# Optimization experiments

Measured on AMD Instinct MI355X. Metric: run time of the kernel, lower is better.

## Reference

```python
import jax, jax.numpy as jnp
import numpy as np

DIM = 1024
H = 16
HD = DIM // H
HIDDEN = 4096
EPS = 1e-5


def layer_norm(x, w, b):
    mu = jnp.mean(x, axis=-1, keepdims=True)
    var = jnp.mean(jnp.square(x - mu), axis=-1, keepdims=True)
    return (x - mu) * jax.lax.rsqrt(var + EPS) * w + b


def setup_inputs() -> dict:
    key = jax.random.key(0)
    ks = jax.random.split(key, 12)
    B, N = 4, 1024
    s = 0.02
    return {
        "x": jax.random.normal(ks[0], (B, N, DIM), jnp.float32),
        "rel_pos_bias": jax.random.normal(ks[1], (H, N, N), jnp.float32) * 0.1,
        "attn_mask": jax.random.randint(ks[2], (B, N), 0, 2, jnp.int32),
        "norm1_w": jnp.ones((DIM,), jnp.float32),
        "norm1_b": jnp.zeros((DIM,), jnp.float32),
        "qkv_w": jax.random.normal(ks[3], (3 * DIM, DIM), jnp.float32) * s,
        "q_bias": jnp.zeros((DIM,), jnp.float32),
        "v_bias": jnp.zeros((DIM,), jnp.float32),
        "proj_w": jax.random.normal(ks[4], (DIM, DIM), jnp.float32) * s,
        "proj_b": jnp.zeros((DIM,), jnp.float32),
        "norm2_w": jnp.ones((DIM,), jnp.float32),
        "norm2_b": jnp.zeros((DIM,), jnp.float32),
        "mlp_w1": jax.random.normal(ks[5], (HIDDEN, DIM), jnp.float32) * s,
        "mlp_b1": jnp.zeros((HIDDEN,), jnp.float32),
        "mlp_w2": jax.random.normal(ks[6], (DIM, HIDDEN), jnp.float32) * s,
        "mlp_b2": jnp.zeros((DIM,), jnp.float32),
    }


def attention(x, rel_pos_bias, attn_mask, qkv_w, q_bias, v_bias, proj_w, proj_b):
    B, N, C = x.shape
    scale = HD ** (-0.5)
    qkv_bias = jnp.concatenate([q_bias, jnp.zeros_like(v_bias), v_bias])
    qkv = x @ qkv_w.T + qkv_bias  # [B,N,3C]
    qkv = qkv.reshape(B, N, 3, H, HD).transpose(2, 0, 3, 1, 4)  # [3,B,H,N,hd]
    q, k, v = qkv[0] * scale, qkv[1], qkv[2]
    attn = jnp.einsum("bhqd,bhkd->bhqk", q, k) + rel_pos_bias[None]
    mask = attn_mask.astype(bool)[:, None, None, :]  # key padding mask
    attn = jnp.where(mask, attn, -jnp.inf)
    attn = jax.nn.softmax(attn, axis=-1)
    out = jnp.einsum("bhqk,bhkd->bhqd", attn, v)
    out = out.transpose(0, 2, 1, 3).reshape(B, N, C)
    return out @ proj_w.T + proj_b


def mlp(x, w1, b1, w2, b2):
    h = jax.nn.gelu(x @ w1.T + b1, approximate=False)
    return h @ w2.T + b2


def reference(x, rel_pos_bias, attn_mask, norm1_w, norm1_b, qkv_w, q_bias, v_bias,
              proj_w, proj_b, norm2_w, norm2_b, mlp_w1, mlp_b1, mlp_w2, mlp_b2):
    # pre-norm block, gamma=None, postnorm=False
    x = x + attention(layer_norm(x, norm1_w, norm1_b), rel_pos_bias, attn_mask,
                      qkv_w, q_bias, v_bias, proj_w, proj_b)
    x = x + mlp(layer_norm(x, norm2_w, norm2_b), mlp_w1, mlp_b1, mlp_w2, mlp_b2)
    return x
```

## Files before the change

### kernel.cpp

```cpp
#include <hip/hip_runtime.h>
#include <math.h>

#define DIM 1024
#define NHEAD 16
#define HD 64
#define HIDDEN 4096
#define SEQ 1024
#define BATCH 4
#define ROWS (BATCH*SEQ)

typedef __attribute__((ext_vector_type(8))) short bf16x8;
typedef __attribute__((ext_vector_type(4))) float f32x4;
typedef __attribute__((ext_vector_type(4))) unsigned short us4;

__device__ __forceinline__ unsigned short f2bf(float f) {
  unsigned u = __builtin_bit_cast(unsigned, f);
  u += 0x7fffu + ((u >> 16) & 1u);
  return (unsigned short)(u >> 16);
}

__device__ __forceinline__ void glds16(const void* g, void* l) {
  __builtin_amdgcn_global_load_lds((const __attribute__((address_space(1))) void*)g,
                                   (__attribute__((address_space(3))) void*)l,
                                   16, 0, 0);
}

__global__ void cvt_all(const float* __restrict__ a, const float* __restrict__ b,
                        const float* __restrict__ c, const float* __restrict__ d,
                        unsigned short* __restrict__ oa, unsigned short* __restrict__ ob,
                        unsigned short* __restrict__ oc, unsigned short* __restrict__ od) {
  const int na = 3 * DIM * DIM / 4, nb = DIM * DIM / 4, nc = HIDDEN * DIM / 4, nd = DIM * HIDDEN / 4;
  const int total = na + nb + nc + nd;
  for (int i = blockIdx.x * blockDim.x + threadIdx.x; i < total; i += gridDim.x * blockDim.x) {
    const float* in; unsigned short* out; int j = i;
    if (j < na)             { in = a; out = oa; }
    else if ((j -= na) < nb){ in = b; out = ob; }
    else if ((j -= nb) < nc){ in = c; out = oc; }
    else                    { j -= nc; in = d; out = od; }
    float4 v = reinterpret_cast<const float4*>(in)[j];
    us4 o = { f2bf(v.x), f2bf(v.y), f2bf(v.z), f2bf(v.w) };
    reinterpret_cast<us4*>(out)[j] = o;
  }
}

__global__ void ln_kernel(const float* __restrict__ x, const float* __restrict__ w,
                          const float* __restrict__ b, unsigned short* __restrict__ out) {
  int row = blockIdx.x;
  const float* xr = x + (size_t)row * DIM;
  int t = threadIdx.x;
  float4 v = *reinterpret_cast<const float4*>(xr + t * 4);
  float s  = v.x + v.y + v.z + v.w;
  float s2 = v.x*v.x + v.y*v.y + v.z*v.z + v.w*v.w;
#pragma unroll
  for (int m = 1; m < 64; m <<= 1) { s += __shfl_xor(s, m); s2 += __shfl_xor(s2, m); }
  __shared__ float red[8];
  int wv = t >> 6, ln = t & 63;
  if (ln == 0) { red[wv] = s; red[4 + wv] = s2; }
  __syncthreads();
  s  = red[0] + red[1] + red[2] + red[3];
  s2 = red[4] + red[5] + red[6] + red[7];
  float mu  = s * (1.0f / DIM);
  float var = s2 * (1.0f / DIM) - mu * mu;
  float rs  = rsqrtf(var + 1e-5f);
  float4 wv4 = *reinterpret_cast<const float4*>(w + t * 4);
  float4 bv4 = *reinterpret_cast<const float4*>(b + t * 4);
  us4 o = { f2bf((v.x - mu) * rs * wv4.x + bv4.x),
            f2bf((v.y - mu) * rs * wv4.y + bv4.y),
            f2bf((v.z - mu) * rs * wv4.z + bv4.z),
            f2bf((v.w - mu) * rs * wv4.w + bv4.w) };
  *reinterpret_cast<us4*>(out + (size_t)row * DIM + t * 4) = o;
}

template<int MODE, int BN>
__global__ __launch_bounds__(256)
void gemm128(const unsigned short* __restrict__ A, const unsigned short* __restrict__ Bw,
             int K, int N,
             const float* __restrict__ bias, const float* __restrict__ resid,
             float* __restrict__ outf, unsigned short* __restrict__ outh,
             unsigned short* __restrict__ qo, unsigned short* __restrict__ ko,
             unsigned short* __restrict__ vto,
             const float* __restrict__ qbias, const float* __restrict__ vbias)
{
  constexpr int NJ = BN / 32;
  __shared__ unsigned short smA[2][128 * 32];
  __shared__ unsigned short smB[2][BN * 32];
  const int tid = threadIdx.x;
  const int wv = tid >> 6, ln = tid & 63;
  const int tile_m = blockIdx.x * 128, tile_n = blockIdx.y * BN;
  const int wm = (wv >> 1) * 64, wn = (wv & 1) * (BN / 2);

  const unsigned short* gA = A  + (size_t)(tile_m + wv * 32 + (ln >> 2)) * K + (ln & 3) * 8;
  const unsigned short* gB = Bw + (size_t)(tile_n + wv * (BN / 4) + (ln >> 2)) * K + (ln & 3) * 8;

  f32x4 acc[4][NJ] = {};
  const int lr = ln & 15, lc8 = (ln >> 4) * 8;

  auto stage = [&](int buf, int k0) {
    glds16(gA + k0,                  &smA[buf][wv * 1024]);
    glds16(gA + k0 + 16 * (size_t)K, &smA[buf][wv * 1024 + 512]);
    glds16(gB + k0,                  &smB[buf][wv * (BN / 4) * 32]);
    if (BN == 128) glds16(gB + k0 + 16 * (size_t)K, &smB[buf][wv * 1024 + 512]);
  };

  stage(0, 0);
  __syncthreads();
  int cur = 0;
  for (int k0 = 0; k0 < K; k0 += 32) {
    if (k0 + 32 < K) stage(cur ^ 1, k0 + 32);
    bf16x8 af[4], bfr[NJ];
#pragma unroll
    for (int i = 0; i < 4; i++)
      af[i] = *reinterpret_cast<const bf16x8*>(&smA[cur][(wm + i * 16 + lr) * 32 + lc8]);
#pragma unroll
    for (int j = 0; j < NJ; j++)
      bfr[j] = *reinterpret_cast<const bf16x8*>(&smB[cur][(wn + j * 16 + lr) * 32 + lc8]);
#pragma unroll
    for (int i = 0; i < 4; i++)
#pragma unroll
      for (int j = 0; j < NJ; j++)
        acc[i][j] = __builtin_amdgcn_mfma_f32_16x16x32_bf16(af[i], bfr[j], acc[i][j], 0, 0, 0);
    __syncthreads();
    cur ^= 1;
  }

  const int lcol = ln & 15, lrow4 = (ln >> 4) * 4;
#pragma unroll
  for (int i = 0; i < 4; i++) {
#pragma unroll
    for (int j = 0; j < NJ; j++) {
      int gm0 = tile_m + wm + i * 16 + lrow4;
      int gn  = tile_n + wn + j * 16 + lcol;
#pragma unroll
      for (int r = 0; r < 4; r++) {
        int gm = gm0 + r;
        float val = acc[i][j][r];
        if (MODE == 0) {
          int b = gm >> 10, n = gm & 1023;
          if (gn < DIM) {
            float q = (val + qbias[gn]) * 0.125f;
            qo[(size_t)((b * NHEAD + (gn >> 6)) * SEQ + n) * HD + (gn & 63)] = f2bf(q);
          } else if (gn < 2 * DIM) {
            int g2 = gn - DIM;
            ko[(size_t)((b * NHEAD + (g2 >> 6)) * SEQ + n) * HD + (g2 & 63)] = f2bf(val);
          } else {
            int g3 = gn - 2 * DIM;
            vto[(size_t)((b * NHEAD + (g3 >> 6)) * HD + (g3 & 63)) * SEQ + n] = f2bf(val + vbias[g3]);
          }
        } else if (MODE == 1) {
          outf[(size_t)gm * N + gn] = val + bias[gn] + resid[(size_t)gm * N + gn];
        } else if (MODE == 2) {
          float t = val + bias[gn];
          float g = 0.5f * t * (1.0f + erff(t * 0.70710678118f));
          outh[(size_t)gm * N + gn] = f2bf(g);
        } else {
          outf[(size_t)gm * N + gn] = val + bias[gn] + resid[(size_t)gm * N + gn];
        }
      }
    }
  }
}

__global__ __launch_bounds__(512)
void attn_kernel(const unsigned short* __restrict__ qg, const unsigned short* __restrict__ kg,
                 const unsigned short* __restrict__ vtg, const float* __restrict__ rpb,
                 const int* __restrict__ amask, unsigned short* __restrict__ outh)
{
  constexpr int PSTR = 72;
  __shared__ unsigned short smK[2][64 * 64];
  __shared__ unsigned short smV[2][64 * 64];
  __shared__ unsigned short pls[8][16 * PSTR];
  const int tid = threadIdx.x;
  const int wv = tid >> 6, ln = tid & 63;
  const int bh = blockIdx.y, b = bh >> 4, h = bh & 15;
  const int q0 = blockIdx.x * 128 + wv * 16;
  const unsigned short* qb = qg  + (size_t)bh * SEQ * HD;
  const unsigned short* kb = kg  + (size_t)bh * SEQ * HD;
  const unsigned short* vb = vtg + (size_t)bh * HD * SEQ;
  const int* mp = amask + b * SEQ;
  unsigned short* myp = pls[wv];

  const int lcol = ln & 15, g = ln >> 4, lc8 = g * 8, lrow4 = g * 4;
  const int sw = (lcol & 7) << 3;
  const float* bprow = rpb + (size_t)h * SEQ * SEQ + (size_t)(q0 + lcol) * SEQ;

  const int srr = ln >> 3;
  const int scc = (ln & 7) ^ srr;

  bf16x8 aq0 = *reinterpret_cast<const bf16x8*>(qb + (size_t)(q0 + lcol) * HD + lc8);
  bf16x8 aq1 = *reinterpret_cast<const bf16x8*>(qb + (size_t)(q0 + lcol) * HD + 32 + lc8);

  f32x4 o[4] = {};
  float m = -1e30f, l = 0.f;

  auto stage = [&](int buf, int kt) {
    int row = wv * 8 + srr;
    glds16(kb + (size_t)(kt + row) * HD + scc * 8, &smK[buf][wv * 512]);
    glds16(vb + (size_t)row * SEQ + kt + scc * 8, &smV[buf][wv * 512]);
  };

  stage(0, 0);
  __syncthreads();

  for (int t = 0; t < SEQ / 64; t++) {
    const int cur = t & 1;
    const int kt = t * 64;
    float4 bv4[4]; int4 mv[4];
#pragma unroll
    for (int j = 0; j < 4; j++) {
      bv4[j] = *reinterpret_cast<const float4*>(bprow + kt + j * 16 + lrow4);
      mv[j]  = *reinterpret_cast<const int4*>(mp + kt + j * 16 + lrow4);
    }
    if (t < SEQ / 64 - 1) stage(cur ^ 1, kt + 64);

    f32x4 s[4];
#pragma unroll
    for (int j = 0; j < 4; j++) {
      int r = j * 16 + lcol;
      bf16x8 bk0 = *reinterpret_cast<const bf16x8*>(&smK[cur][r * 64 + (lc8 ^ sw)]);
      bf16x8 bk1 = *reinterpret_cast<const bf16x8*>(&smK[cur][r * 64 + ((32 + lc8) ^ sw)]);
      f32x4 z = {0.f, 0.f, 0.f, 0.f};
      z = __builtin_amdgcn_mfma_f32_16x16x32_bf16(bk0, aq0, z, 0, 0, 0);
      z = __builtin_amdgcn_mfma_f32_16x16x32_bf16(bk1, aq1, z, 0, 0, 0);
      s[j] = z;
    }
#pragma unroll
    for (int j = 0; j < 4; j++) {
      s[j][0] = mv[j].x ? s[j][0] + bv4[j].x : -1e30f;
      s[j][1] = mv[j].y ? s[j][1] + bv4[j].y : -1e30f;
      s[j][2] = mv[j].z ? s[j][2] + bv4[j].z : -1e30f;
      s[j][3] = mv[j].w ? s[j][3] + bv4[j].w : -1e30f;
    }
    float pm = fmaxf(fmaxf(fmaxf(s[0][0], s[0][1]), fmaxf(s[0][2], s[0][3])),
                     fmaxf(fmaxf(s[1][0], s[1][1]), fmaxf(s[1][2], s[1][3])));
    pm = fmaxf(pm, fmaxf(fmaxf(fmaxf(s[2][0], s[2][1]), fmaxf(s[2][2], s[2][3])),
                         fmaxf(fmaxf(s[3][0], s[3][1]), fmaxf(s[3][2], s[3][3]))));
    pm = fmaxf(pm, __shfl_xor(pm, 16));
    pm = fmaxf(pm, __shfl_xor(pm, 32));
    float mn = fmaxf(m, pm);
    float fr = __expf(m - mn);
    m = mn;
    float rs = 0.f;
#pragma unroll
    for (int j = 0; j < 4; j++)
#pragma unroll
      for (int r = 0; r < 4; r++) {
        float p = __expf(s[j][r] - m);
        s[j][r] = p;
        rs += p;
      }
    rs += __shfl_xor(rs, 16);
    rs += __shfl_xor(rs, 32);
    l = l * fr + rs;
    float frq[4];
#pragma unroll
    for (int r = 0; r < 4; r++) frq[r] = __shfl(fr, lrow4 + r);
#pragma unroll
    for (int d = 0; d < 4; d++)
#pragma unroll
      for (int r = 0; r < 4; r++) o[d][r] *= frq[r];
#pragma unroll
    for (int j = 0; j < 4; j++) {
      us4 po = { f2bf(s[j][0]), f2bf(s[j][1]), f2bf(s[j][2]), f2bf(s[j][3]) };
      *reinterpret_cast<us4*>(myp + lcol * PSTR + j * 16 + lrow4) = po;
    }
    asm volatile("s_waitcnt lgkmcnt(0)" ::: "memory");
    __builtin_amdgcn_sched_barrier(0);
#pragma unroll
    for (int c = 0; c < 2; c++) {
      bf16x8 ap = *reinterpret_cast<const bf16x8*>(myp + lcol * PSTR + c * 32 + lc8);
#pragma unroll
      for (int d = 0; d < 4; d++) {
        int vr = d * 16 + lcol;
        bf16x8 bvv = *reinterpret_cast<const bf16x8*>(&smV[cur][vr * 64 + ((c * 32 + lc8) ^ sw)]);
        o[d] = __builtin_amdgcn_mfma_f32_16x16x32_bf16(ap, bvv, o[d], 0, 0, 0);
      }
    }
    __syncthreads();
  }
  float linv = 1.0f / l;
  float lq[4];
#pragma unroll
  for (int r = 0; r < 4; r++) lq[r] = __shfl(linv, lrow4 + r);
#pragma unroll
  for (int d = 0; d < 4; d++)
#pragma unroll
    for (int r = 0; r < 4; r++)
      outh[(size_t)(b * SEQ + q0 + lrow4 + r) * DIM + h * HD + d * 16 + lcol] = f2bf(o[d][r] * lq[r]);
}

extern "C" void kernel_launch(void* const* d_in, const int* in_sizes, int n_in,
                              void* d_out, int out_size, void* d_ws, size_t ws_size,
                              hipStream_t stream)
{
  const float* x      = (const float*)d_in[0];
  const float* rpb    = (const float*)d_in[1];
  const int*   amask  = (const int*)d_in[2];
  const float* n1w    = (const float*)d_in[3];
  const float* n1b    = (const float*)d_in[4];
  const float* qkv_w  = (const float*)d_in[5];
  const float* q_bias = (const float*)d_in[6];
  const float* v_bias = (const float*)d_in[7];
  const float* proj_w = (const float*)d_in[8];
  const float* proj_b = (const float*)d_in[9];
  const float* n2w    = (const float*)d_in[10];
  const float* n2b    = (const float*)d_in[11];
  const float* w1     = (const float*)d_in[12];
  const float* b1     = (const float*)d_in[13];
  const float* w2     = (const float*)d_in[14];
  const float* b2     = (const float*)d_in[15];
  float* out = (float*)d_out;

  char* ws = (char*)d_ws;
  size_t off = 0;
  auto alloc = [&](size_t bytes) { char* p = ws + off; off += (bytes + 255) & ~(size_t)255; return p; };
  unsigned short* xn1    = (unsigned short*)alloc((size_t)ROWS * DIM * 2);
  unsigned short* xn2    = (unsigned short*)alloc((size_t)ROWS * DIM * 2);
  unsigned short* wqkv_h = (unsigned short*)alloc((size_t)3 * DIM * DIM * 2);
  unsigned short* wproj_h= (unsigned short*)alloc((size_t)DIM * DIM * 2);
  unsigned short* w1_h   = (unsigned short*)alloc((size_t)HIDDEN * DIM * 2);
  unsigned short* w2_h   = (unsigned short*)alloc((size_t)DIM * HIDDEN * 2);
  unsigned short* qh     = (unsigned short*)alloc((size_t)ROWS * DIM * 2);
  unsigned short* kh     = (unsigned short*)alloc((size_t)ROWS * DIM * 2);
  unsigned short* vth    = (unsigned short*)alloc((size_t)ROWS * DIM * 2);
  unsigned short* attn_h = (unsigned short*)alloc((size_t)ROWS * DIM * 2);
  float*          xres   = (float*)alloc((size_t)ROWS * DIM * 4);
  unsigned short* hmid   = (unsigned short*)alloc((size_t)ROWS * HIDDEN * 2);

  cvt_all<<<2048, 256, 0, stream>>>(qkv_w, proj_w, w1, w2, wqkv_h, wproj_h, w1_h, w2_h);

  ln_kernel<<<ROWS, 256, 0, stream>>>(x, n1w, n1b, xn1);
  gemm128<0, 128><<<dim3(ROWS / 128, 3 * DIM / 128), 256, 0, stream>>>(
      xn1, wqkv_h, DIM, 3 * DIM, nullptr, nullptr, nullptr, nullptr, qh, kh, vth, q_bias, v_bias);
  attn_kernel<<<dim3(SEQ / 128, BATCH * NHEAD), 512, 0, stream>>>(qh, kh, vth, rpb, amask, attn_h);
  gemm128<1, 64><<<dim3(ROWS / 128, DIM / 64), 256, 0, stream>>>(
      attn_h, wproj_h, DIM, DIM, proj_b, x, xres, nullptr, nullptr, nullptr, nullptr, nullptr, nullptr);
  ln_kernel<<<ROWS, 256, 0, stream>>>(xres, n2w, n2b, xn2);
  gemm128<2, 128><<<dim3(ROWS / 128, HIDDEN / 128), 256, 0, stream>>>(
      xn2, w1_h, DIM, HIDDEN, b1, nullptr, nullptr, hmid, nullptr, nullptr, nullptr, nullptr, nullptr);
  gemm128<3, 64><<<dim3(ROWS / 128, DIM / 64), 256, 0, stream>>>(
      hmid, w2_h, HIDDEN, DIM, b2, xres, out, nullptr, nullptr, nullptr, nullptr, nullptr, nullptr);
}
```

Baseline: 308.4 us.

## Triple-buffer GEMM loads and prefetch attention bias/mask one tile ahead

The GEMM moves from double to triple LDS buffering. It issues loads two k-steps ahead and replaces the per-iteration __syncthreads with one s_barrier plus explicit vmcnt waits, so global_load_lds traffic overlaps more MFMA work. The attention kernel now prefetches the next tile's rel-pos bias and mask into registers, drops the trailing __syncthreads in favour of a barrier at the top of the loop, and raises wave priority around the MFMA sections. One risk: the vmcnt wait follows the barrier, so a wave only waits on its own loads before reading LDS that other waves staged, which may be a cross-wave race. The extra buffer also adds LDS and register pressure.

```diff
diff --git a/kernel.cpp b/kernel.cpp
--- a/kernel.cpp
+++ b/kernel.cpp
@@ -82,8 +82,9 @@
              const float* __restrict__ qbias, const float* __restrict__ vbias)
 {
   constexpr int NJ = BN / 32;
-  __shared__ unsigned short smA[2][128 * 32];
-  __shared__ unsigned short smB[2][BN * 32];
+  constexpr int GL = (BN == 128) ? 4 : 3;
+  __shared__ unsigned short smA[3][128 * 32];
+  __shared__ unsigned short smB[3][BN * 32];
   const int tid = threadIdx.x;
   const int wv = tid >> 6, ln = tid & 63;
   const int tile_m = blockIdx.x * 128, tile_n = blockIdx.y * BN;
@@ -103,10 +104,21 @@
   };
 
   stage(0, 0);
-  __syncthreads();
+  stage(1, 32);
   int cur = 0;
   for (int k0 = 0; k0 < K; k0 += 32) {
-    if (k0 + 32 < K) stage(cur ^ 1, k0 + 32);
+    __builtin_amdgcn_s_barrier();
+    __builtin_amdgcn_sched_barrier(0);
+    if (k0 + 64 < K) {
+      int nb = cur - 1; if (nb < 0) nb += 3;
+      stage(nb, k0 + 64);
+      asm volatile("s_waitcnt vmcnt(%0)" :: "i"(2 * GL) : "memory");
+    } else if (k0 + 32 < K) {
+      asm volatile("s_waitcnt vmcnt(%0)" :: "i"(GL) : "memory");
+    } else {
+      asm volatile("s_waitcnt vmcnt(0)" ::: "memory");
+    }
+    __builtin_amdgcn_sched_barrier(0);
     bf16x8 af[4], bfr[NJ];
 #pragma unroll
     for (int i = 0; i < 4; i++)
@@ -119,8 +131,7 @@
 #pragma unroll
       for (int j = 0; j < NJ; j++)
         acc[i][j] = __builtin_amdgcn_mfma_f32_16x16x32_bf16(af[i], bfr[j], acc[i][j], 0, 0, 0);
-    __syncthreads();
-    cur ^= 1;
+    cur = (cur == 2) ? 0 : cur + 1;
   }
 
   const int lcol = ln & 15, lrow4 = (ln >> 4) * 4;
@@ -166,6 +177,7 @@
                  const int* __restrict__ amask, unsigned short* __restrict__ outh)
 {
   constexpr int PSTR = 72;
+  constexpr int NT = SEQ / 64;
   __shared__ unsigned short smK[2][64 * 64];
   __shared__ unsigned short smV[2][64 * 64];
   __shared__ unsigned short pls[8][16 * PSTR];
@@ -198,21 +210,36 @@
     glds16(vb + (size_t)row * SEQ + kt + scc * 8, &smV[buf][wv * 512]);
   };
 
+  float4 bcur[4]; int4 mcur[4];
+  float4 bnxt[4]; int4 mnxt[4];
+
   stage(0, 0);
-  __syncthreads();
-
-  for (int t = 0; t < SEQ / 64; t++) {
+#pragma unroll
+  for (int j = 0; j < 4; j++) {
+    bcur[j] = *reinterpret_cast<const float4*>(bprow + j * 16 + lrow4);
+    mcur[j] = *reinterpret_cast<const int4*>(mp + j * 16 + lrow4);
+  }
+
+  for (int t = 0; t < NT; t++) {
     const int cur = t & 1;
     const int kt = t * 64;
-    float4 bv4[4]; int4 mv[4];
-#pragma unroll
-    for (int j = 0; j < 4; j++) {
-      bv4[j] = *reinterpret_cast<const float4*>(bprow + kt + j * 16 + lrow4);
-      mv[j]  = *reinterpret_cast<const int4*>(mp + kt + j * 16 + lrow4);
-    }
-    if (t < SEQ / 64 - 1) stage(cur ^ 1, kt + 64);
+    __builtin_amdgcn_s_barrier();
+    __builtin_amdgcn_sched_barrier(0);
+    if (t + 1 < NT) {
+      stage(cur ^ 1, kt + 64);
+#pragma unroll
+      for (int j = 0; j < 4; j++) {
+        bnxt[j] = *reinterpret_cast<const float4*>(bprow + kt + 64 + j * 16 + lrow4);
+        mnxt[j] = *reinterpret_cast<const int4*>(mp + kt + 64 + j * 16 + lrow4);
+      }
+      asm volatile("s_waitcnt vmcnt(10)" ::: "memory");
+    } else {
+      asm volatile("s_waitcnt vmcnt(0)" ::: "memory");
+    }
+    __builtin_amdgcn_sched_barrier(0);
 
     f32x4 s[4];
+    __builtin_amdgcn_s_setprio(1);
 #pragma unroll
     for (int j = 0; j < 4; j++) {
       int r = j * 16 + lcol;
@@ -223,12 +250,13 @@
       z = __builtin_amdgcn_mfma_f32_16x16x32_bf16(bk1, aq1, z, 0, 0, 0);
       s[j] = z;
     }
+    __builtin_amdgcn_s_setprio(0);
 #pragma unroll
     for (int j = 0; j < 4; j++) {
-      s[j][0] = mv[j].x ? s[j][0] + bv4[j].x : -1e30f;
-      s[j][1] = mv[j].y ? s[j][1] + bv4[j].y : -1e30f;
-      s[j][2] = mv[j].z ? s[j][2] + bv4[j].z : -1e30f;
-      s[j][3] = mv[j].w ? s[j][3] + bv4[j].w : -1e30f;
+      s[j][0] = mcur[j].x ? s[j][0] + bcur[j].x : -1e30f;
+      s[j][1] = mcur[j].y ? s[j][1] + bcur[j].y : -1e30f;
+      s[j][2] = mcur[j].z ? s[j][2] + bcur[j].z : -1e30f;
+      s[j][3] = mcur[j].w ? s[j][3] + bcur[j].w : -1e30f;
     }
     float pm = fmaxf(fmaxf(fmaxf(s[0][0], s[0][1]), fmaxf(s[0][2], s[0][3])),
                      fmaxf(fmaxf(s[1][0], s[1][1]), fmaxf(s[1][2], s[1][3])));
@@ -265,6 +293,7 @@
     }
     asm volatile("s_waitcnt lgkmcnt(0)" ::: "memory");
     __builtin_amdgcn_sched_barrier(0);
+    __builtin_amdgcn_s_setprio(1);
 #pragma unroll
     for (int c = 0; c < 2; c++) {
       bf16x8 ap = *reinterpret_cast<const bf16x8*>(myp + lcol * PSTR + c * 32 + lc8);
@@ -275,7 +304,11 @@
         o[d] = __builtin_amdgcn_mfma_f32_16x16x32_bf16(ap, bvv, o[d], 0, 0, 0);
       }
     }
-    __syncthreads();
+    __builtin_amdgcn_s_setprio(0);
+    if (t + 1 < NT) {
+#pragma unroll
+      for (int j = 0; j < 4; j++) { bcur[j] = bnxt[j]; mcur[j] = mnxt[j]; }
+    }
   }
   float linv = 1.0f / l;
   float lq[4];
```

Result: slower. 331.2 us (+7.4%).

## Load attention K/V fragments directly from global memory and skip rescales lazily

Applied to the files above, without the earlier changes.

The attention kernel stops staging K and V tiles in LDS with double buffering and block barriers. Each wave now loads its K and V MFMA fragments straight from global memory into registers, and the block shrinks to 4 waves covering 64 queries. It also adds lazy online-softmax rescaling that skips the max update and output rescale when the new max exceeds the old by at most 8, and uses s_setprio around the MFMA sections. This removes the LDS traffic and __syncthreads, but each wave now re-reads K/V from global or L2 with less reuse across the block.

```diff
diff --git a/kernel.cpp b/kernel.cpp
--- a/kernel.cpp
+++ b/kernel.cpp
@@ -160,19 +160,17 @@
   }
 }
 
-__global__ __launch_bounds__(512)
+__global__ __launch_bounds__(256)
 void attn_kernel(const unsigned short* __restrict__ qg, const unsigned short* __restrict__ kg,
                  const unsigned short* __restrict__ vtg, const float* __restrict__ rpb,
                  const int* __restrict__ amask, unsigned short* __restrict__ outh)
 {
   constexpr int PSTR = 72;
-  __shared__ unsigned short smK[2][64 * 64];
-  __shared__ unsigned short smV[2][64 * 64];
-  __shared__ unsigned short pls[8][16 * PSTR];
+  __shared__ unsigned short pls[4][16 * PSTR];
   const int tid = threadIdx.x;
   const int wv = tid >> 6, ln = tid & 63;
   const int bh = blockIdx.y, b = bh >> 4, h = bh & 15;
-  const int q0 = blockIdx.x * 128 + wv * 16;
+  const int q0 = blockIdx.x * 64 + wv * 16;
   const unsigned short* qb = qg  + (size_t)bh * SEQ * HD;
   const unsigned short* kb = kg  + (size_t)bh * SEQ * HD;
   const unsigned short* vb = vtg + (size_t)bh * HD * SEQ;
@@ -180,11 +178,7 @@
   unsigned short* myp = pls[wv];
 
   const int lcol = ln & 15, g = ln >> 4, lc8 = g * 8, lrow4 = g * 4;
-  const int sw = (lcol & 7) << 3;
   const float* bprow = rpb + (size_t)h * SEQ * SEQ + (size_t)(q0 + lcol) * SEQ;
-
-  const int srr = ln >> 3;
-  const int scc = (ln & 7) ^ srr;
 
   bf16x8 aq0 = *reinterpret_cast<const bf16x8*>(qb + (size_t)(q0 + lcol) * HD + lc8);
   bf16x8 aq1 = *reinterpret_cast<const bf16x8*>(qb + (size_t)(q0 + lcol) * HD + 32 + lc8);
@@ -192,37 +186,33 @@
   f32x4 o[4] = {};
   float m = -1e30f, l = 0.f;
 
-  auto stage = [&](int buf, int kt) {
-    int row = wv * 8 + srr;
-    glds16(kb + (size_t)(kt + row) * HD + scc * 8, &smK[buf][wv * 512]);
-    glds16(vb + (size_t)row * SEQ + kt + scc * 8, &smV[buf][wv * 512]);
-  };
-
-  stage(0, 0);
-  __syncthreads();
-
-  for (int t = 0; t < SEQ / 64; t++) {
-    const int cur = t & 1;
-    const int kt = t * 64;
+  for (int kt = 0; kt < SEQ; kt += 64) {
+    bf16x8 kf0[4], kf1[4];
     float4 bv4[4]; int4 mv[4];
 #pragma unroll
     for (int j = 0; j < 4; j++) {
+      const unsigned short* kp = kb + (size_t)(kt + j * 16 + lcol) * HD + lc8;
+      kf0[j] = *reinterpret_cast<const bf16x8*>(kp);
+      kf1[j] = *reinterpret_cast<const bf16x8*>(kp + 32);
       bv4[j] = *reinterpret_cast<const float4*>(bprow + kt + j * 16 + lrow4);
       mv[j]  = *reinterpret_cast<const int4*>(mp + kt + j * 16 + lrow4);
     }
-    if (t < SEQ / 64 - 1) stage(cur ^ 1, kt + 64);
-
     f32x4 s[4];
+    __builtin_amdgcn_s_setprio(1);
 #pragma unroll
     for (int j = 0; j < 4; j++) {
-      int r = j * 16 + lcol;
-      bf16x8 bk0 = *reinterpret_cast<const bf16x8*>(&smK[cur][r * 64 + (lc8 ^ sw)]);
-      bf16x8 bk1 = *reinterpret_cast<const bf16x8*>(&smK[cur][r * 64 + ((32 + lc8) ^ sw)]);
       f32x4 z = {0.f, 0.f, 0.f, 0.f};
-      z = __builtin_amdgcn_mfma_f32_16x16x32_bf16(bk0, aq0, z, 0, 0, 0);
-      z = __builtin_amdgcn_mfma_f32_16x16x32_bf16(bk1, aq1, z, 0, 0, 0);
+      z = __builtin_amdgcn_mfma_f32_16x16x32_bf16(kf0[j], aq0, z, 0, 0, 0);
+      z = __builtin_amdgcn_mfma_f32_16x16x32_bf16(kf1[j], aq1, z, 0, 0, 0);
       s[j] = z;
     }
+    __builtin_amdgcn_s_setprio(0);
+    bf16x8 vf[2][4];
+#pragma unroll
+    for (int c = 0; c < 2; c++)
+#pragma unroll
+      for (int d = 0; d < 4; d++)
+        vf[c][d] = *reinterpret_cast<const bf16x8*>(vb + (size_t)(d * 16 + lcol) * SEQ + kt + c * 32 + lc8);
 #pragma unroll
     for (int j = 0; j < 4; j++) {
       s[j][0] = mv[j].x ? s[j][0] + bv4[j].x : -1e30f;
@@ -236,9 +226,19 @@
                          fmaxf(fmaxf(s[3][0], s[3][1]), fmaxf(s[3][2], s[3][3]))));
     pm = fmaxf(pm, __shfl_xor(pm, 16));
     pm = fmaxf(pm, __shfl_xor(pm, 32));
-    float mn = fmaxf(m, pm);
-    float fr = __expf(m - mn);
-    m = mn;
+    if (!__all(pm - m <= 8.0f)) {
+      float mn = fmaxf(m, pm);
+      float fr = __expf(m - mn);
+      m = mn;
+      l *= fr;
+      float frq[4];
+#pragma unroll
+      for (int r = 0; r < 4; r++) frq[r] = __shfl(fr, lrow4 + r);
+#pragma unroll
+      for (int d = 0; d < 4; d++)
+#pragma unroll
+        for (int r = 0; r < 4; r++) o[d][r] *= frq[r];
+    }
     float rs = 0.f;
 #pragma unroll
     for (int j = 0; j < 4; j++)
@@ -250,14 +250,7 @@
       }
     rs += __shfl_xor(rs, 16);
     rs += __shfl_xor(rs, 32);
-    l = l * fr + rs;
-    float frq[4];
-#pragma unroll
-    for (int r = 0; r < 4; r++) frq[r] = __shfl(fr, lrow4 + r);
-#pragma unroll
-    for (int d = 0; d < 4; d++)
-#pragma unroll
-      for (int r = 0; r < 4; r++) o[d][r] *= frq[r];
+    l += rs;
 #pragma unroll
     for (int j = 0; j < 4; j++) {
       us4 po = { f2bf(s[j][0]), f2bf(s[j][1]), f2bf(s[j][2]), f2bf(s[j][3]) };
@@ -265,17 +258,15 @@
     }
     asm volatile("s_waitcnt lgkmcnt(0)" ::: "memory");
     __builtin_amdgcn_sched_barrier(0);
+    __builtin_amdgcn_s_setprio(1);
 #pragma unroll
     for (int c = 0; c < 2; c++) {
       bf16x8 ap = *reinterpret_cast<const bf16x8*>(myp + lcol * PSTR + c * 32 + lc8);
 #pragma unroll
-      for (int d = 0; d < 4; d++) {
-        int vr = d * 16 + lcol;
-        bf16x8 bvv = *reinterpret_cast<const bf16x8*>(&smV[cur][vr * 64 + ((c * 32 + lc8) ^ sw)]);
-        o[d] = __builtin_amdgcn_mfma_f32_16x16x32_bf16(ap, bvv, o[d], 0, 0, 0);
-      }
-    }
-    __syncthreads();
+      for (int d = 0; d < 4; d++)
+        o[d] = __builtin_amdgcn_mfma_f32_16x16x32_bf16(ap, vf[c][d], o[d], 0, 0, 0);
+    }
+    __builtin_amdgcn_s_setprio(0);
   }
   float linv = 1.0f / l;
   float lq[4];
@@ -331,7 +322,7 @@
   ln_kernel<<<ROWS, 256, 0, stream>>>(x, n1w, n1b, xn1);
   gemm128<0, 128><<<dim3(ROWS / 128, 3 * DIM / 128), 256, 0, stream>>>(
       xn1, wqkv_h, DIM, 3 * DIM, nullptr, nullptr, nullptr, nullptr, qh, kh, vth, q_bias, v_bias);
-  attn_kernel<<<dim3(SEQ / 128, BATCH * NHEAD), 512, 0, stream>>>(qh, kh, vth, rpb, amask, attn_h);
+  attn_kernel<<<dim3(SEQ / 64, BATCH * NHEAD), 256, 0, stream>>>(qh, kh, vth, rpb, amask, attn_h);
   gemm128<1, 64><<<dim3(ROWS / 128, DIM / 64), 256, 0, stream>>>(
       attn_h, wproj_h, DIM, DIM, proj_b, x, xres, nullptr, nullptr, nullptr, nullptr, nullptr, nullptr);
   ln_kernel<<<ROWS, 256, 0, stream>>>(xres, n2w, n2b, xn2);
```

Result: slower. 393.1 us (+27.4%).
